# Optimization experiments

Measured on AMD Instinct MI355X. Metric: run time of the kernel, lower is better.

## Reference

```python
import jax, jax.numpy as jnp
import numpy as np

TEMPERATURE = 2.0 / 3.0
LIMIT_A = -0.1
LIMIT_B = 1.1

N_NODES = 50000
N_CLUSTERS = 64
N_RELATIONS = 8
N_EDGES = 1000000


def setup_inputs() -> dict:
    key = jax.random.key(0)
    ks = jax.random.split(key, 6)
    xavier = float(np.sqrt(6.0 / (N_CLUSTERS + N_CLUSTERS)))
    return {
        "assignments": jax.random.normal(ks[0], (N_NODES, N_CLUSTERS), jnp.float32),
        "inter_cluster_logits": jax.random.uniform(ks[1], (N_RELATIONS, N_CLUSTERS, N_CLUSTERS), jnp.float32, -xavier, xavier),
        "log_alpha": jnp.zeros((N_RELATIONS, N_CLUSTERS, N_CLUSTERS), jnp.float32),
        "absent_bias": jnp.zeros((N_RELATIONS,), jnp.float32),
        "edge_index": jax.random.randint(ks[2], (2, N_EDGES), 0, N_NODES, jnp.int32),
        "edge_type": jax.random.randint(ks[3], (N_EDGES,), 0, N_RELATIONS, jnp.int32),
        "neg_edge_index": jax.random.randint(ks[4], (2, N_EDGES), 0, N_NODES, jnp.int32),
        "neg_edge_type": jax.random.randint(ks[5], (N_EDGES,), 0, N_RELATIONS, jnp.int32),
    }


def _edge_logits(assignments, weights, absent_bias, edge_index, edge_type):
    # src, dst: [E, C] gathers (irregular access)
    src = assignments[edge_index[0]]
    dst = assignments[edge_index[1]]
    n_rel = weights.shape[0]
    # torch.bmm(W[et], dst[:, :, None]) == dst @ W[et].T ; compute per relation
    # (fixed small relation loop; avoids materializing [E, C, C]) then select.
    logits_all = jnp.stack(
        [jnp.sum(src * (dst @ weights[r].T), axis=-1) for r in range(n_rel)],
        axis=-1,
    )  # [E, R]
    logits = jnp.take_along_axis(logits_all, edge_type[:, None], axis=1)[:, 0]
    return logits + absent_bias[edge_type]


def reference(assignments, inter_cluster_logits, log_alpha, absent_bias,
              edge_index, edge_type, neg_edge_index, neg_edge_type):
    # Hard-concrete gate, eval mode: z = clamp(sigmoid(log_alpha)*(b-a)+a, 0, 1)
    gate = jnp.clip(jax.nn.sigmoid(log_alpha) * (LIMIT_B - LIMIT_A) + LIMIT_A, 0.0, 1.0)
    weights = jax.nn.sigmoid(inter_cluster_logits) * gate  # [R, C, C]

    pos_logits = _edge_logits(assignments, weights, absent_bias, edge_index, edge_type)
    neg_logits = _edge_logits(assignments, weights, absent_bias, neg_edge_index, neg_edge_type)

    # BCE-with-logits: target=1 -> softplus(-x); target=0 -> softplus(x)
    pos_loss = jnp.mean(jax.nn.softplus(-pos_logits))
    neg_loss = jnp.mean(jax.nn.softplus(neg_logits))
    return pos_loss + neg_loss
```

## Files before the change

### kernel.cpp

```cpp
#include <hip/hip_runtime.h>
#include <hip/hip_bf16.h>
#include <math.h>

#define E_EDGES 1000000
#define N_NODES 50000
#define N_C     64
#define N_REL   8
#define CHB     1024
#define CAP     192
#define NBLK    977
#define BT      256
#define SENT    0xFFFFFFFFu

typedef __attribute__((ext_vector_type(4))) float floatx4;
typedef __attribute__((ext_vector_type(2))) float floatx2;

static __device__ __forceinline__ unsigned pk4_fp8(float a, float b, float c, float d) {
    unsigned w = 0;
    w = __builtin_amdgcn_cvt_pk_fp8_f32(a, b, w, false);
    w = __builtin_amdgcn_cvt_pk_fp8_f32(c, d, w, true);
    return w;
}

static __device__ __forceinline__ long long pack64(unsigned lo, unsigned hi) {
    uint2 u; u.x = lo; u.y = hi;
    return __builtin_bit_cast(long long, u);
}

__global__ __launch_bounds__(256) void prep_kernel(
    const float* __restrict__ assign,
    const float* __restrict__ icl,
    const float* __restrict__ la,
    unsigned char* __restrict__ Wp8,
    unsigned char* __restrict__ AS8,
    float* __restrict__ out)
{
    int tid = blockIdx.x * blockDim.x + threadIdx.x;
    int nth = gridDim.x * blockDim.x;
    if (tid == 0) out[0] = 0.0f;

    for (int idx = tid; idx < N_REL * N_C * 16; idx += nth) {
        int row = idx >> 4, dq = idx & 15;
        int q = dq >> 2, c = (dq >> 1) & 1, jh = dq & 1;
        int k0 = (2 * c + jh) * 16 + 4 * q;
        float wv[4];
        #pragma unroll
        for (int b = 0; b < 4; ++b) {
            int srci = (row << 6) + k0 + b;
            float w = 1.0f / (1.0f + __expf(-icl[srci]));
            float g = 1.0f / (1.0f + __expf(-la[srci])) * 1.2f - 0.1f;
            g = fminf(fmaxf(g, 0.0f), 1.0f);
            wv[b] = w * g;
        }
        ((unsigned*)Wp8)[idx] = pk4_fp8(wv[0], wv[1], wv[2], wv[3]);
    }

    for (int n = tid; n < N_NODES; n += nth) {
        const float4* a4 = (const float4*)(assign + (size_t)n * N_C);
        unsigned w[16];
        #pragma unroll
        for (int i = 0; i < 16; ++i) {
            float4 v = a4[i];
            w[i] = pk4_fp8(v.x, v.y, v.z, v.w);
        }
        uint4* as = (uint4*)(AS8 + (size_t)n * N_C);
        #pragma unroll
        for (int q = 0; q < 4; ++q) {
            uint4 o;
            o.x = w[0 * 4 + q];
            o.y = w[1 * 4 + q];
            o.z = w[2 * 4 + q];
            o.w = w[3 * 4 + q];
            as[q] = o;
        }
    }
}

__global__ __launch_bounds__(BT, 4) void edge_kernel(
    const unsigned char* __restrict__ AS8,
    const unsigned char* __restrict__ Wp8,
    const float* __restrict__ absent_bias,
    const int* __restrict__ ei, const int* __restrict__ et,
    const int* __restrict__ nei, const int* __restrict__ net,
    float* __restrict__ out)
{
    __shared__ uint4 Wl4[N_REL * N_C * 4];
    __shared__ unsigned list[N_REL * CAP];
    __shared__ float bias_l[N_REL];
    __shared__ unsigned cnt[N_REL];
    __shared__ float red[4];
    if (threadIdx.x < N_REL) {
        cnt[threadIdx.x] = 0u;
        bias_l[threadIdx.x] = absent_bias[threadIdx.x];
    }

    {
        const uint4* Wg = (const uint4*)Wp8;
        #pragma unroll
        for (int k = 0; k < 8; ++k) {
            int e = threadIdx.x + k * BT;
            Wl4[e ^ ((e >> 2) & 7)] = Wg[e];
        }
    }

    int blk = blockIdx.x;
    bool isneg = blk >= NBLK;
    int lb = isneg ? blk - NBLK : blk;
    const int* Es = isneg ? nei : ei;
    const int* Et = isneg ? net : et;
    float sign = isneg ? 1.0f : -1.0f;
    int base = lb * CHB;
    int elim = min(base + CHB, E_EDGES);

    __syncthreads();

    {
        int e0 = base + threadIdx.x;
        int sv[4], dv[4], rv[4];
        bool mv[4];
        #pragma unroll
        for (int k = 0; k < 4; ++k) {
            int e = e0 + k * BT;
            mv[k] = e < elim;
            int ec = mv[k] ? e : base;
            sv[k] = __builtin_nontemporal_load(&Es[ec]);
            dv[k] = __builtin_nontemporal_load(&Es[E_EDGES + ec]);
            rv[k] = __builtin_nontemporal_load(&Et[ec]);
        }
        #pragma unroll
        for (int k = 0; k < 4; ++k) {
            if (mv[k]) {
                unsigned rank = atomicAdd(&cnt[rv[k]], 1u);
                if (rank < CAP)
                    list[rv[k] * CAP + rank] = (unsigned)sv[k] | ((unsigned)dv[k] << 16);
            }
        }
    }
    __syncthreads();

    if (threadIdx.x < N_REL * 16) {
        int r = threadIdx.x >> 4;
        int i = threadIdx.x & 15;
        int n = min((int)cnt[r], CAP);
        int padded = ((n + 15) >> 4) << 4;
        int slot = n + i;
        if (slot < padded) list[r * CAP + slot] = SENT;
    }
    __syncthreads();

    int lane = threadIdx.x & 63;
    int wid  = __builtin_amdgcn_readfirstlane(threadIdx.x >> 6);
    int n16  = lane & 15;
    int quad = lane >> 4;
    float loss = 0.0f;

    int G0 = __builtin_amdgcn_readfirstlane((min((int)cnt[0], CAP) + 15) >> 4);
    int G1 = __builtin_amdgcn_readfirstlane((min((int)cnt[1], CAP) + 15) >> 4);
    int G2 = __builtin_amdgcn_readfirstlane((min((int)cnt[2], CAP) + 15) >> 4);
    int G3 = __builtin_amdgcn_readfirstlane((min((int)cnt[3], CAP) + 15) >> 4);
    int G4 = __builtin_amdgcn_readfirstlane((min((int)cnt[4], CAP) + 15) >> 4);
    int G5 = __builtin_amdgcn_readfirstlane((min((int)cnt[5], CAP) + 15) >> 4);
    int G6 = __builtin_amdgcn_readfirstlane((min((int)cnt[6], CAP) + 15) >> 4);
    int G7 = __builtin_amdgcn_readfirstlane((min((int)cnt[7], CAP) + 15) >> 4);
    int go1 = G0;
    int go2 = go1 + G1;
    int go3 = go2 + G2;
    int go4 = go3 + G3;
    int go5 = go4 + G4;
    int go6 = go5 + G5;
    int go7 = go6 + G6;
    int tg  = go7 + G7;
    int tgm1 = tg - 1;

    #define LOCATE(ITEM, R, GOF)                                   \
        do {                                                       \
            R = 0; GOF = 0;                                        \
            if ((ITEM) >= go1) { R = 1; GOF = go1; }               \
            if ((ITEM) >= go2) { R = 2; GOF = go2; }               \
            if ((ITEM) >= go3) { R = 3; GOF = go3; }               \
            if ((ITEM) >= go4) { R = 4; GOF = go4; }               \
            if ((ITEM) >= go5) { R = 5; GOF = go5; }               \
            if ((ITEM) >= go6) { R = 6; GOF = go6; }               \
            if ((ITEM) >= go7) { R = 7; GOF = go7; }               \
        } while (0)

    #define ISSUE(VIT, RECV, SREG, DREG, WF0, WF1, WF2, WF3, BI)             \
        do {                                                                 \
            int vc_ = (VIT) < tgm1 ? (VIT) : tgm1;                           \
            int r_, gof_;                                                    \
            LOCATE(vc_, r_, gof_);                                           \
            unsigned recr_ = list[r_ * CAP + (vc_ - gof_) * 16 + n16];       \
            RECV = (VIT) < end ? recr_ : SENT;                               \
            unsigned sm_ = RECV != SENT ? (RECV & 0xFFFFu) : 0u;             \
            unsigned dm_ = RECV != SENT ? (RECV >> 16) : 0u;                 \
            SREG = *(const uint4*)(AS8 + ((size_t)sm_ << 6) + quad * 16);    \
            DREG = *(const uint4*)(AS8 + ((size_t)dm_ << 6) + quad * 16);    \
            int rb_ = r_ * 64 + n16;                                         \
            {                                                                \
                int row0_ = rb_;                                             \
                WF0 = Wl4[(row0_ * 4 + quad) ^ (row0_ & 7)];                 \
                int row1_ = rb_ + 16;                                        \
                WF1 = Wl4[(row1_ * 4 + quad) ^ (row1_ & 7)];                 \
                int row2_ = rb_ + 32;                                        \
                WF2 = Wl4[(row2_ * 4 + quad) ^ (row2_ & 7)];                 \
                int row3_ = rb_ + 48;                                        \
                WF3 = Wl4[(row3_ * 4 + quad) ^ (row3_ & 7)];                 \
            }                                                                \
            BI = bias_l[r_];                                                 \
        } while (0)

    #define COMPUTE(RECV, SS, DD, WF0, WF1, WF2, WF3, BI)                    \
        do {                                                                 \
            long long bD0 = pack64((DD).x, (DD).y);                          \
            long long bD1 = pack64((DD).z, (DD).w);                          \
            unsigned sw0 = (SS).x, sw1 = (SS).y, sw2 = (SS).z, sw3 = (SS).w; \
            float d0 = 0.0f, d1 = 0.0f;                                      \
            {                                                                \
                floatx4 p0 = zero4, p1 = zero4;                              \
                p0 = __builtin_amdgcn_mfma_f32_16x16x32_fp8_fp8(             \
                        pack64((WF0).x, (WF0).y), bD0, p0, 0, 0, 0);         \
                p1 = __builtin_amdgcn_mfma_f32_16x16x32_fp8_fp8(             \
                        pack64((WF1).x, (WF1).y), bD0, p1, 0, 0, 0);         \
                p0 = __builtin_amdgcn_mfma_f32_16x16x32_fp8_fp8(             \
                        pack64((WF0).z, (WF0).w), bD1, p0, 0, 0, 0);         \
                p1 = __builtin_amdgcn_mfma_f32_16x16x32_fp8_fp8(             \
                        pack64((WF1).z, (WF1).w), bD1, p1, 0, 0, 0);         \
                floatx2 lo0 = __builtin_amdgcn_cvt_pk_f32_fp8((int)sw0, false);\
                floatx2 hi0 = __builtin_amdgcn_cvt_pk_f32_fp8((int)sw0, true);\
                floatx2 lo1 = __builtin_amdgcn_cvt_pk_f32_fp8((int)sw1, false);\
                floatx2 hi1 = __builtin_amdgcn_cvt_pk_f32_fp8((int)sw1, true);\
                d0 = fmaf(lo0.x, p0[0], d0); d1 = fmaf(lo1.x, p1[0], d1);    \
                d0 = fmaf(lo0.y, p0[1], d0); d1 = fmaf(lo1.y, p1[1], d1);    \
                d0 = fmaf(hi0.x, p0[2], d0); d1 = fmaf(hi1.x, p1[2], d1);    \
                d0 = fmaf(hi0.y, p0[3], d0); d1 = fmaf(hi1.y, p1[3], d1);    \
            }                                                                \
            {                                                                \
                floatx4 p0 = zero4, p1 = zero4;                              \
                p0 = __builtin_amdgcn_mfma_f32_16x16x32_fp8_fp8(             \
                        pack64((WF2).x, (WF2).y), bD0, p0, 0, 0, 0);         \
                p1 = __builtin_amdgcn_mfma_f32_16x16x32_fp8_fp8(             \
                        pack64((WF3).x, (WF3).y), bD0, p1, 0, 0, 0);         \
                p0 = __builtin_amdgcn_mfma_f32_16x16x32_fp8_fp8(             \
                        pack64((WF2).z, (WF2).w), bD1, p0, 0, 0, 0);         \
                p1 = __builtin_amdgcn_mfma_f32_16x16x32_fp8_fp8(             \
                        pack64((WF3).z, (WF3).w), bD1, p1, 0, 0, 0);         \
                floatx2 lo0 = __builtin_amdgcn_cvt_pk_f32_fp8((int)sw2, false);\
                floatx2 hi0 = __builtin_amdgcn_cvt_pk_f32_fp8((int)sw2, true);\
                floatx2 lo1 = __builtin_amdgcn_cvt_pk_f32_fp8((int)sw3, false);\
                floatx2 hi1 = __builtin_amdgcn_cvt_pk_f32_fp8((int)sw3, true);\
                d0 = fmaf(lo0.x, p0[0], d0); d1 = fmaf(lo1.x, p1[0], d1);    \
                d0 = fmaf(lo0.y, p0[1], d0); d1 = fmaf(lo1.y, p1[1], d1);    \
                d0 = fmaf(hi0.x, p0[2], d0); d1 = fmaf(hi1.x, p1[2], d1);    \
                d0 = fmaf(hi0.y, p0[3], d0); d1 = fmaf(hi1.y, p1[3], d1);    \
            }                                                                \
            float dot = d0 + d1;                                             \
            dot += __shfl_xor(dot, 16);                                      \
            dot += __shfl_xor(dot, 32);                                      \
            float x = sign * (dot + (BI));                                   \
            float sp = fmaxf(x, 0.0f) + __logf(1.0f + __expf(-fabsf(x)));    \
            bool live = (quad == 0) && (RECV != SENT);                       \
            loss += live ? sp : 0.0f;                                        \
        } while (0)

    int start = (wid * tg) >> 2;
    int end   = ((wid + 1) * tg) >> 2;

    const floatx4 zero4 = {0.0f, 0.0f, 0.0f, 0.0f};

    if (start < end) {
        unsigned recA, recB, recC;
        uint4 SA, DA, SB, DB, SC, DC;
        uint4 wA0, wA1, wA2, wA3, wB0, wB1, wB2, wB3, wC0, wC1, wC2, wC3;
        float bA, bB, bC;

        int vA = start, vB = start + 1, vC = start + 2;
        ISSUE(vA, recA, SA, DA, wA0, wA1, wA2, wA3, bA);
        ISSUE(vB, recB, SB, DB, wB0, wB1, wB2, wB3, bB);
        ISSUE(vC, recC, SC, DC, wC0, wC1, wC2, wC3, bC);

        int n3 = (end - start + 2) / 3;
        #pragma clang loop unroll(disable)
        for (int k = 0; k < n3; ++k) {
            COMPUTE(recA, SA, DA, wA0, wA1, wA2, wA3, bA);
            vA += 3;
            ISSUE(vA, recA, SA, DA, wA0, wA1, wA2, wA3, bA);

            COMPUTE(recB, SB, DB, wB0, wB1, wB2, wB3, bB);
            vB += 3;
            ISSUE(vB, recB, SB, DB, wB0, wB1, wB2, wB3, bB);

            COMPUTE(recC, SC, DC, wC0, wC1, wC2, wC3, bC);
            vC += 3;
            ISSUE(vC, recC, SC, DC, wC0, wC1, wC2, wC3, bC);
        }
    }

    loss += __shfl_xor(loss, 1);
    loss += __shfl_xor(loss, 2);
    loss += __shfl_xor(loss, 4);
    loss += __shfl_xor(loss, 8);
    loss += __shfl_xor(loss, 16);
    loss += __shfl_xor(loss, 32);
    if (lane == 0) red[wid] = loss;
    __syncthreads();
    if (threadIdx.x == 0) {
        float t = red[0] + red[1] + red[2] + red[3];
        atomicAdd(out, t * (1.0f / (float)E_EDGES));
    }
}

extern "C" void kernel_launch(void* const* d_in, const int* in_sizes, int n_in,
                              void* d_out, int out_size, void* d_ws, size_t ws_size,
                              hipStream_t stream) {
    const float* assign = (const float*)d_in[0];
    const float* icl    = (const float*)d_in[1];
    const float* la     = (const float*)d_in[2];
    const float* ab     = (const float*)d_in[3];
    const int*   ei     = (const int*)d_in[4];
    const int*   et     = (const int*)d_in[5];
    const int*   nei    = (const int*)d_in[6];
    const int*   net    = (const int*)d_in[7];
    float* out = (float*)d_out;

    char* basep = (char*)d_ws;
    unsigned char* Wp8 = (unsigned char*)basep;
    unsigned char* AS8 = (unsigned char*)(basep + 65536);

    prep_kernel<<<256, 256, 0, stream>>>(assign, icl, la, Wp8, AS8, out);
    edge_kernel<<<2 * NBLK, BT, 0, stream>>>(AS8, Wp8, ab, ei, et, nei, net, out);
}
```

Measured before the change: 137.1 us.

## Bucket edges by source-node block so source rows are read from LDS

Adds a scatter kernel that uses global atomics to bin all positive and negative edges into per-64-source-node buckets, packing dst, local src offset and relation into one word. The edge kernel then loads that block's 64 source rows into LDS once and gathers only destination rows from global memory. The aim is to remove half of the random global row gathers. In exchange it adds a full extra pass over the edge indices, a bucket write/read and heavily contended global atomics. The change also drops the LDS XOR swizzle on the weights, adds sched_barriers between pipeline stages, and lowers the occupancy hint from 4 to 3.

```diff
diff --git a/kernel.cpp b/kernel.cpp
--- a/kernel.cpp
+++ b/kernel.cpp
@@ -6,9 +6,9 @@
 #define N_NODES 50000
 #define N_C     64
 #define N_REL   8
-#define CHB     1024
-#define CAP     192
-#define NBLK    977
+#define NBK     782
+#define BCAP    1536
+#define CAP2    256
 #define BT      256
 #define SENT    0xFFFFFFFFu
 
@@ -33,11 +33,14 @@
     const float* __restrict__ la,
     unsigned char* __restrict__ Wp8,
     unsigned char* __restrict__ AS8,
+    unsigned* __restrict__ gcnt,
     float* __restrict__ out)
 {
     int tid = blockIdx.x * blockDim.x + threadIdx.x;
     int nth = gridDim.x * blockDim.x;
     if (tid == 0) out[0] = 0.0f;
+
+    for (int i = tid; i < 2 * NBK * 16; i += nth) gcnt[i] = 0u;
 
     for (int idx = tid; idx < N_REL * N_C * 16; idx += nth) {
         int row = idx >> 4, dq = idx & 15;
@@ -76,19 +79,44 @@
     }
 }
 
-__global__ __launch_bounds__(BT, 4) void edge_kernel(
+__global__ __launch_bounds__(256) void scatter_kernel(
+    const int* __restrict__ ei, const int* __restrict__ et,
+    const int* __restrict__ nei, const int* __restrict__ net,
+    unsigned* __restrict__ buckets, unsigned* __restrict__ gcnt)
+{
+    int tid = blockIdx.x * blockDim.x + threadIdx.x;
+    int nth = gridDim.x * blockDim.x;
+    for (int e = tid; e < 2 * E_EDGES; e += nth) {
+        bool isneg = e >= E_EDGES;
+        int idx = isneg ? e - E_EDGES : e;
+        const int* Es = isneg ? nei : ei;
+        const int* Et = isneg ? net : et;
+        int s = __builtin_nontemporal_load(&Es[idx]);
+        int d = __builtin_nontemporal_load(&Es[E_EDGES + idx]);
+        int r = __builtin_nontemporal_load(&Et[idx]);
+        int b = (s >> 6) + (isneg ? NBK : 0);
+        unsigned pos = atomicAdd(&gcnt[b * 16], 1u);
+        if (pos < BCAP)
+            buckets[(size_t)b * BCAP + pos] =
+                (unsigned)d | ((unsigned)(s & 63) << 16) | ((unsigned)r << 22);
+    }
+}
+
+__global__ __launch_bounds__(BT, 3) void edge_kernel(
     const unsigned char* __restrict__ AS8,
     const unsigned char* __restrict__ Wp8,
     const float* __restrict__ absent_bias,
-    const int* __restrict__ ei, const int* __restrict__ et,
-    const int* __restrict__ nei, const int* __restrict__ net,
+    const unsigned* __restrict__ buckets,
+    const unsigned* __restrict__ gcnt,
     float* __restrict__ out)
 {
-    __shared__ uint4 Wl4[N_REL * N_C * 4];
-    __shared__ unsigned list[N_REL * CAP];
+    __shared__ uint4 Wl[N_REL * 64 * 4];
+    __shared__ uint4 Sl[64 * 4];
+    __shared__ unsigned list[N_REL * CAP2];
     __shared__ float bias_l[N_REL];
     __shared__ unsigned cnt[N_REL];
     __shared__ float red[4];
+
     if (threadIdx.x < N_REL) {
         cnt[threadIdx.x] = 0u;
         bias_l[threadIdx.x] = absent_bias[threadIdx.x];
@@ -99,52 +127,40 @@
         #pragma unroll
         for (int k = 0; k < 8; ++k) {
             int e = threadIdx.x + k * BT;
-            Wl4[e ^ ((e >> 2) & 7)] = Wg[e];
-        }
-    }
-
-    int blk = blockIdx.x;
-    bool isneg = blk >= NBLK;
-    int lb = isneg ? blk - NBLK : blk;
-    const int* Es = isneg ? nei : ei;
-    const int* Et = isneg ? net : et;
+            Wl[e] = Wg[e];
+        }
+    }
+
+    int b = blockIdx.x;
+    bool isneg = b >= NBK;
+    int node0 = (isneg ? b - NBK : b) << 6;
     float sign = isneg ? 1.0f : -1.0f;
-    int base = lb * CHB;
-    int elim = min(base + CHB, E_EDGES);
-
+
+    {
+        int row = threadIdx.x >> 2, q = threadIdx.x & 3;
+        int node = node0 + row;
+        node = node < N_NODES ? node : N_NODES - 1;
+        Sl[threadIdx.x] = *(const uint4*)(AS8 + ((size_t)node << 6) + q * 16);
+    }
     __syncthreads();
 
-    {
-        int e0 = base + threadIdx.x;
-        int sv[4], dv[4], rv[4];
-        bool mv[4];
-        #pragma unroll
-        for (int k = 0; k < 4; ++k) {
-            int e = e0 + k * BT;
-            mv[k] = e < elim;
-            int ec = mv[k] ? e : base;
-            sv[k] = __builtin_nontemporal_load(&Es[ec]);
-            dv[k] = __builtin_nontemporal_load(&Es[E_EDGES + ec]);
-            rv[k] = __builtin_nontemporal_load(&Et[ec]);
-        }
-        #pragma unroll
-        for (int k = 0; k < 4; ++k) {
-            if (mv[k]) {
-                unsigned rank = atomicAdd(&cnt[rv[k]], 1u);
-                if (rank < CAP)
-                    list[rv[k] * CAP + rank] = (unsigned)sv[k] | ((unsigned)dv[k] << 16);
-            }
-        }
+    int nb = min((int)gcnt[b * 16], BCAP);
+
+    for (int i = threadIdx.x; i < nb; i += BT) {
+        unsigned rec = buckets[(size_t)b * BCAP + i];
+        int r = (rec >> 22) & 7;
+        unsigned rank = atomicAdd(&cnt[r], 1u);
+        if (rank < CAP2) list[r * CAP2 + rank] = rec & 0x3FFFFFu;
     }
     __syncthreads();
 
     if (threadIdx.x < N_REL * 16) {
         int r = threadIdx.x >> 4;
         int i = threadIdx.x & 15;
-        int n = min((int)cnt[r], CAP);
+        int n = min((int)cnt[r], CAP2);
         int padded = ((n + 15) >> 4) << 4;
         int slot = n + i;
-        if (slot < padded) list[r * CAP + slot] = SENT;
+        if (slot < padded) list[r * CAP2 + slot] = SENT;
     }
     __syncthreads();
 
@@ -154,14 +170,14 @@
     int quad = lane >> 4;
     float loss = 0.0f;
 
-    int G0 = __builtin_amdgcn_readfirstlane((min((int)cnt[0], CAP) + 15) >> 4);
-    int G1 = __builtin_amdgcn_readfirstlane((min((int)cnt[1], CAP) + 15) >> 4);
-    int G2 = __builtin_amdgcn_readfirstlane((min((int)cnt[2], CAP) + 15) >> 4);
-    int G3 = __builtin_amdgcn_readfirstlane((min((int)cnt[3], CAP) + 15) >> 4);
-    int G4 = __builtin_amdgcn_readfirstlane((min((int)cnt[4], CAP) + 15) >> 4);
-    int G5 = __builtin_amdgcn_readfirstlane((min((int)cnt[5], CAP) + 15) >> 4);
-    int G6 = __builtin_amdgcn_readfirstlane((min((int)cnt[6], CAP) + 15) >> 4);
-    int G7 = __builtin_amdgcn_readfirstlane((min((int)cnt[7], CAP) + 15) >> 4);
+    int G0 = __builtin_amdgcn_readfirstlane((min((int)cnt[0], CAP2) + 15) >> 4);
+    int G1 = __builtin_amdgcn_readfirstlane((min((int)cnt[1], CAP2) + 15) >> 4);
+    int G2 = __builtin_amdgcn_readfirstlane((min((int)cnt[2], CAP2) + 15) >> 4);
+    int G3 = __builtin_amdgcn_readfirstlane((min((int)cnt[3], CAP2) + 15) >> 4);
+    int G4 = __builtin_amdgcn_readfirstlane((min((int)cnt[4], CAP2) + 15) >> 4);
+    int G5 = __builtin_amdgcn_readfirstlane((min((int)cnt[5], CAP2) + 15) >> 4);
+    int G6 = __builtin_amdgcn_readfirstlane((min((int)cnt[6], CAP2) + 15) >> 4);
+    int G7 = __builtin_amdgcn_readfirstlane((min((int)cnt[7], CAP2) + 15) >> 4);
     int go1 = G0;
     int go2 = go1 + G1;
     int go3 = go2 + G2;
@@ -189,23 +205,17 @@
             int vc_ = (VIT) < tgm1 ? (VIT) : tgm1;                           \
             int r_, gof_;                                                    \
             LOCATE(vc_, r_, gof_);                                           \
-            unsigned recr_ = list[r_ * CAP + (vc_ - gof_) * 16 + n16];       \
+            unsigned recr_ = list[r_ * CAP2 + (vc_ - gof_) * 16 + n16];      \
             RECV = (VIT) < end ? recr_ : SENT;                               \
-            unsigned sm_ = RECV != SENT ? (RECV & 0xFFFFu) : 0u;             \
-            unsigned dm_ = RECV != SENT ? (RECV >> 16) : 0u;                 \
-            SREG = *(const uint4*)(AS8 + ((size_t)sm_ << 6) + quad * 16);    \
+            unsigned dm_ = RECV != SENT ? (RECV & 0xFFFFu) : 0u;             \
+            unsigned slo_ = RECV != SENT ? ((RECV >> 16) & 63u) : 0u;        \
             DREG = *(const uint4*)(AS8 + ((size_t)dm_ << 6) + quad * 16);    \
+            SREG = Sl[slo_ * 4 + quad];                                      \
             int rb_ = r_ * 64 + n16;                                         \
-            {                                                                \
-                int row0_ = rb_;                                             \
-                WF0 = Wl4[(row0_ * 4 + quad) ^ (row0_ & 7)];                 \
-                int row1_ = rb_ + 16;                                        \
-                WF1 = Wl4[(row1_ * 4 + quad) ^ (row1_ & 7)];                 \
-                int row2_ = rb_ + 32;                                        \
-                WF2 = Wl4[(row2_ * 4 + quad) ^ (row2_ & 7)];                 \
-                int row3_ = rb_ + 48;                                        \
-                WF3 = Wl4[(row3_ * 4 + quad) ^ (row3_ & 7)];                 \
-            }                                                                \
+            WF0 = Wl[(rb_) * 4 + quad];                                      \
+            WF1 = Wl[(rb_ + 16) * 4 + quad];                                 \
+            WF2 = Wl[(rb_ + 32) * 4 + quad];                                 \
+            WF3 = Wl[(rb_ + 48) * 4 + quad];                                 \
             BI = bias_l[r_];                                                 \
         } while (0)
 
@@ -277,6 +287,7 @@
         ISSUE(vA, recA, SA, DA, wA0, wA1, wA2, wA3, bA);
         ISSUE(vB, recB, SB, DB, wB0, wB1, wB2, wB3, bB);
         ISSUE(vC, recC, SC, DC, wC0, wC1, wC2, wC3, bC);
+        __builtin_amdgcn_sched_barrier(0);
 
         int n3 = (end - start + 2) / 3;
         #pragma clang loop unroll(disable)
@@ -284,14 +295,17 @@
             COMPUTE(recA, SA, DA, wA0, wA1, wA2, wA3, bA);
             vA += 3;
             ISSUE(vA, recA, SA, DA, wA0, wA1, wA2, wA3, bA);
+            __builtin_amdgcn_sched_barrier(0);
 
             COMPUTE(recB, SB, DB, wB0, wB1, wB2, wB3, bB);
             vB += 3;
             ISSUE(vB, recB, SB, DB, wB0, wB1, wB2, wB3, bB);
+            __builtin_amdgcn_sched_barrier(0);
 
             COMPUTE(recC, SC, DC, wC0, wC1, wC2, wC3, bC);
             vC += 3;
             ISSUE(vC, recC, SC, DC, wC0, wC1, wC2, wC3, bC);
+            __builtin_amdgcn_sched_barrier(0);
         }
     }
 
@@ -325,7 +339,10 @@
     char* basep = (char*)d_ws;
     unsigned char* Wp8 = (unsigned char*)basep;
     unsigned char* AS8 = (unsigned char*)(basep + 65536);
-
-    prep_kernel<<<256, 256, 0, stream>>>(assign, icl, la, Wp8, AS8, out);
-    edge_kernel<<<2 * NBLK, BT, 0, stream>>>(AS8, Wp8, ab, ei, et, nei, net, out);
-}
+    unsigned* buckets  = (unsigned*)(basep + 3265536);
+    unsigned* gcnt     = (unsigned*)(basep + 12874752);
+
+    prep_kernel<<<256, 256, 0, stream>>>(assign, icl, la, Wp8, AS8, gcnt, out);
+    scatter_kernel<<<2048, 256, 0, stream>>>(ei, et, nei, net, buckets, gcnt);
+    edge_kernel<<<2 * NBK, BT, 0, stream>>>(AS8, Wp8, ab, buckets, gcnt, out);
+}
```

After: 237.4 us. +73.1%, slower.
